# Performance work log

Measured on AMD Instinct MI355X. Metric: run time of the kernel, lower is better.

The kernel has to match this reference:

```python
import jax, jax.numpy as jnp
import numpy as np

N, E = 50000, 1600000
IN_CH, HEADS, OUT_PER_HEAD = 128, 4, 32  # out_channels=128 // 4 heads
NEG_SLOPE = 0.2


def setup_inputs() -> dict:
    key = jax.random.key(0)
    ks = jax.random.split(key, 10)
    HC = HEADS * OUT_PER_HEAD
    glorot = lambda k, shape: jax.random.uniform(k, shape, jnp.float32, -1.0, 1.0) * jnp.sqrt(6.0 / (shape[0] + shape[-1]))
    return {
        "x": jax.random.normal(ks[0], (N, IN_CH), jnp.float32),
        "edge_index": jax.random.randint(ks[1], (2, E), 0, N),
        "edge_weight": jax.random.uniform(ks[2], (E,), jnp.float32),
        "Wl": glorot(ks[3], (IN_CH, HC)),
        "bl": jnp.zeros((HC,), jnp.float32),
        "Wr": glorot(ks[4], (IN_CH, HC)),
        "br": jnp.zeros((HC,), jnp.float32),
        "We": glorot(ks[5], (1, HC)),           # lin_edge, bias=False
        "att": glorot(ks[6], (HEADS, OUT_PER_HEAD)),
        "bias": jnp.zeros((HC,), jnp.float32),
    }


def reference(x, edge_index, edge_weight, Wl, bl, Wr, br, We, att, bias):
    n = x.shape[0]
    H, C = att.shape
    src, dst = edge_index[0], edge_index[1]
    # add_self_loops with fill_value='max': self-loop edge_attr = max incoming edge weight per node (0 if none)
    loop_attr = jax.ops.segment_max(edge_weight, dst, num_segments=n)
    loop_attr = jnp.where(jnp.isfinite(loop_attr), loop_attr, 0.0)
    loop = jnp.arange(n)
    src_f = jnp.concatenate([src, loop])
    dst_f = jnp.concatenate([dst, loop])
    ea_f = jnp.concatenate([edge_weight, loop_attr])[:, None]  # [E+N, 1]
    # GATv2: separate src/dst linear transforms
    x_l = (x @ Wl + bl).reshape(n, H, C)
    x_r = (x @ Wr + br).reshape(n, H, C)
    e = (ea_f @ We).reshape(-1, H, C)
    # per-edge message and attention score
    m = jax.nn.leaky_relu(x_l[src_f] + x_r[dst_f] + e, NEG_SLOPE)  # [E+N, H, C]
    alpha = jnp.einsum('ehc,hc->eh', m, att)
    # scatter-softmax over incoming edges per destination node
    amax = jax.ops.segment_max(alpha, dst_f, num_segments=n)
    amax = jnp.where(jnp.isfinite(amax), amax, 0.0)
    aexp = jnp.exp(alpha - amax[dst_f])
    asum = jax.ops.segment_sum(aexp, dst_f, num_segments=n)
    alpha = aexp / (asum[dst_f] + 1e-16)
    # weighted aggregate of source-transformed features
    out = jax.ops.segment_sum(x_l[src_f] * alpha[..., None], dst_f, num_segments=n)
    return out.reshape(n, H * C) + bias
```

## Files before the change

kernel.cpp:

```cpp
#include <hip/hip_runtime.h>
#include <cstdint>

#define NEG 0.2f
#define BSH 4
#define BNODES 16
#define CAP 768
#define EPT 3
#define SBSH 9
#define SBN 512
#define CCAP 18000
#define CCHUNK 3328
#define CEPT 13
#define FSLICE 8
#define LOG2E 1.44269504088896f

typedef __attribute__((ext_vector_type(8))) short short8v;
typedef __attribute__((ext_vector_type(4))) float f32x4;

__device__ __forceinline__ unsigned short f2bf(float f) {
  unsigned u = __float_as_uint(f);
  return (unsigned short)((u + 0x7FFFu + ((u >> 16) & 1u)) >> 16);
}
__device__ __forceinline__ float bf2f(unsigned short h) {
  return __uint_as_float(((unsigned)h) << 16);
}

__global__ __launch_bounds__(256) void k_prep(const float* __restrict__ Wl,
    const float* __restrict__ Wr, const float* __restrict__ We,
    const float* __restrict__ att, unsigned short* __restrict__ WtB,
    float* __restrict__ qe) {
  int mat = blockIdx.x;
  const float* W = mat ? Wr : Wl;
  for (int i = threadIdx.x; i < 16384; i += 256) {
    int c = i >> 7, k = i & 127;
    WtB[mat * 16384 + c * 128 + k] = f2bf(W[k * 128 + c]);
  }
  if (mat == 0) {
    __shared__ float tmp[128];
    if (threadIdx.x < 128) tmp[threadIdx.x] = att[threadIdx.x] * We[threadIdx.x];
    __syncthreads();
    if (threadIdx.x < 4) {
      float s = 0.f;
      for (int c = 0; c < 32; ++c) s += tmp[threadIdx.x * 32 + c];
      qe[threadIdx.x] = 0.6f * LOG2E * s;
    }
  }
}

__global__ __launch_bounds__(256) void k_gemm(const float* __restrict__ x,
    const unsigned short* __restrict__ WtB, const float* __restrict__ att,
    const float* __restrict__ bl, const float* __restrict__ br,
    unsigned short* __restrict__ xlb, unsigned short* __restrict__ xrb,
    float* __restrict__ ql, float* __restrict__ qr, int n) {
  __shared__ __align__(16) unsigned short xs[64][136];
  __shared__ __align__(16) unsigned short Wt[128][136];
  int tid = threadIdx.x;
  int B0 = blockIdx.x * 64;
  int mat = blockIdx.y;
  for (int i = tid; i < 64 * 32; i += 256) {
    int r = i >> 5, c4 = (i & 31) * 4;
    ushort4 o = {0, 0, 0, 0};
    if (B0 + r < n) {
      float4 v = *(const float4*)(x + (size_t)(B0 + r) * 128 + c4);
      o = make_ushort4(f2bf(v.x), f2bf(v.y), f2bf(v.z), f2bf(v.w));
    }
    *(ushort4*)&xs[r][c4] = o;
  }
  for (int i = tid; i < 128 * 32; i += 256) {
    int c = i >> 5, k4 = (i & 31) * 4;
    *(ushort4*)&Wt[c][k4] = *(const ushort4*)(WtB + (size_t)mat * 16384 + c * 128 + k4);
  }
  __syncthreads();
  int wv = tid >> 6, lane = tid & 63;
  int l15 = lane & 15, g = lane >> 4;
  int R0 = wv * 16;
  f32x4 acc[8];
  #pragma unroll
  for (int t = 0; t < 8; ++t) acc[t] = {0.f, 0.f, 0.f, 0.f};
  #pragma unroll
  for (int kc = 0; kc < 4; ++kc) {
    int k0 = kc * 32 + g * 8;
    short8v b = *(const short8v*)&xs[R0 + l15][k0];
    #pragma unroll
    for (int t = 0; t < 8; ++t) {
      short8v a = *(const short8v*)&Wt[t * 16 + l15][k0];
      acc[t] = __builtin_amdgcn_mfma_f32_16x16x32_bf16(a, b, acc[t], 0, 0, 0);
    }
  }
  const float* bias = mat ? br : bl;
  unsigned short* yp = mat ? xrb : xlb;
  float* qdst = mat ? qr : ql;
  int row = B0 + R0 + l15;
  float qp[4] = {0.f, 0.f, 0.f, 0.f};
  if (row < n) {
    const float s06 = 0.6f * LOG2E;
    #pragma unroll
    for (int t = 0; t < 8; ++t) {
      int c0 = t * 16 + g * 4;
      float4 bv = *(const float4*)(bias + c0);
      float4 av = *(const float4*)(att + c0);
      ushort4 o = {f2bf(acc[t][0] + bv.x), f2bf(acc[t][1] + bv.y),
                   f2bf(acc[t][2] + bv.z), f2bf(acc[t][3] + bv.w)};
      *(ushort4*)(yp + (size_t)row * 128 + c0) = o;
      float dot = av.x * bf2f(o.x) + av.y * bf2f(o.y)
                + av.z * bf2f(o.z) + av.w * bf2f(o.w);
      qp[t >> 1] += s06 * dot;
    }
  }
  #pragma unroll
  for (int h = 0; h < 4; ++h) {
    qp[h] += __shfl_xor(qp[h], 16);
    qp[h] += __shfl_xor(qp[h], 32);
  }
  if (row < n && g == 0)
    *(float4*)(qdst + (size_t)row * 4) = make_float4(qp[0], qp[1], qp[2], qp[3]);
}

__global__ __launch_bounds__(256) void k_coarse(const int* __restrict__ eidx,
    const float* __restrict__ ew, unsigned* __restrict__ gsb,
    int2* __restrict__ csb, int E, int NSB) {
  __shared__ unsigned cnt[128];
  __shared__ unsigned base[128];
  int c0 = blockIdx.x * CCHUNK;
  int c1 = min(E, c0 + CCHUNK);
  if (c0 >= c1) return;
  for (int b = threadIdx.x; b < NSB; b += 256) cnt[b] = 0u;
  __syncthreads();
  unsigned dreg[CEPT];
  #pragma unroll
  for (int k = 0; k < CEPT; ++k) {
    int i = c0 + threadIdx.x + k * 256;
    unsigned d = 0u;
    if (i < c1) {
      d = (unsigned)eidx[E + i];
      atomicAdd(&cnt[d >> SBSH], 1u);
    }
    dreg[k] = d;
  }
  __syncthreads();
  for (int b = threadIdx.x; b < NSB; b += 256) {
    unsigned c = cnt[b];
    base[b] = c ? atomicAdd(&gsb[b], c) : 0u;
    cnt[b] = 0u;
  }
  __syncthreads();
  #pragma unroll
  for (int k = 0; k < CEPT; ++k) {
    int i = c0 + threadIdx.x + k * 256;
    if (i < c1) {
      unsigned d = dreg[k];
      unsigned b = d >> SBSH;
      unsigned slot = base[b] + atomicAdd(&cnt[b], 1u);
      if (slot < CCAP)
        csb[(size_t)b * CCAP + slot] =
            make_int2((eidx[i] << SBSH) | (int)(d & (SBN - 1)), __float_as_int(ew[i]));
    }
  }
}

__global__ __launch_bounds__(256) void k_fine(const unsigned* __restrict__ gsb,
    const int2* __restrict__ csb, int2* __restrict__ ebkt,
    unsigned* __restrict__ fcnt, int NB) {
  __shared__ unsigned cnt[32];
  __shared__ unsigned base[32];
  int sb = blockIdx.x / FSLICE;
  int sl = blockIdx.x % FSLICE;
  int ne = min((int)gsb[sb], CCAP);
  int chunk = (ne + FSLICE - 1) / FSLICE;
  int i0 = sl * chunk, i1 = min(ne, i0 + chunk);
  if (i0 >= i1) return;
  const int2* src = csb + (size_t)sb * CCAP;
  if (threadIdx.x < 32) cnt[threadIdx.x] = 0u;
  __syncthreads();
  for (int i = i0 + threadIdx.x; i < i1; i += 256)
    atomicAdd(&cnt[(src[i].x >> 4) & 31], 1u);
  __syncthreads();
  if (threadIdx.x < 32) {
    unsigned c = cnt[threadIdx.x];
    base[threadIdx.x] = c ? atomicAdd(&fcnt[sb * 32 + (int)threadIdx.x], c) : 0u;
    cnt[threadIdx.x] = 0u;
  }
  __syncthreads();
  for (int i = i0 + threadIdx.x; i < i1; i += 256) {
    int2 e = src[i];
    int fb = (e.x >> 4) & 31;
    unsigned slot = base[fb] + atomicAdd(&cnt[fb], 1u);
    if (slot < CAP) {
      int packed = ((e.x >> SBSH) << 4) | (e.x & 15);
      ebkt[(size_t)(sb * 32 + fb) * CAP + slot] = make_int2(packed, e.y);
    }
  }
}

__global__ __launch_bounds__(256) void k_agg(
    const unsigned* __restrict__ fcnt, const int2* __restrict__ ebkt,
    const unsigned short* __restrict__ xlb, const unsigned short* __restrict__ xrb,
    const float* __restrict__ ql, const float* __restrict__ qr,
    const float* __restrict__ qe, const float* __restrict__ We,
    const float* __restrict__ att, const float* __restrict__ bias,
    float* __restrict__ out, int n) {
  __shared__ int2 es[CAP];
  __shared__ unsigned rp[BNODES + 1];
  __shared__ unsigned cur[BNODES];
  __shared__ unsigned scnt[BNODES];
  int tid = threadIdx.x;
  int lane = tid & 63, wv = tid >> 6;
  int bkt = blockIdx.x;
  int ne = min((int)fcnt[bkt], CAP);
  const int2* srcp = ebkt + (size_t)bkt * CAP;
  if (tid < BNODES) scnt[tid] = 0u;
  __syncthreads();
  int2 er[EPT];
  #pragma unroll
  for (int k = 0; k < EPT; ++k) {
    int i = tid + k * 256;
    if (i < ne) {
      er[k] = srcp[i];
      atomicAdd(&scnt[er[k].x & (BNODES - 1)], 1u);
    }
  }
  __syncthreads();
  if (tid < 64) {
    unsigned s = (lane < BNODES) ? scnt[lane] : 0u;
    #pragma unroll
    for (int off = 1; off < BNODES; off <<= 1) {
      unsigned t = __shfl_up(s, off);
      if (lane >= off) s += t;
    }
    if (lane < BNODES) { rp[lane + 1] = s; cur[lane] = 0u; }
    if (lane == 0) rp[0] = 0u;
  }
  __syncthreads();
  #pragma unroll
  for (int k = 0; k < EPT; ++k) {
    int i = tid + k * 256;
    if (i < ne) {
      int dl = er[k].x & (BNODES - 1);
      unsigned slot = rp[dl] + atomicAdd(&cur[dl], 1u);
      es[slot] = make_int2(er[k].x >> BSH, er[k].y);
    }
  }
  __syncthreads();

  int g = lane >> 4;
  int l4 = lane & 15;
  int h = l4 >> 2;
  int ch0 = l4 * 8;
  float4 weA = *(const float4*)(We + ch0);
  float4 weB = *(const float4*)(We + ch0 + 4);
  float4 atA = *(const float4*)(att + ch0);
  float4 atB = *(const float4*)(att + ch0 + 4);
  const float s04 = 0.4f * LOG2E;
  atA.x *= s04; atA.y *= s04; atA.z *= s04; atA.w *= s04;
  atB.x *= s04; atB.y *= s04; atB.z *= s04; atB.w *= s04;
  float qeh = qe[h];

  for (int dl = wv; dl < BNODES; dl += 4) {
    int d = (bkt << BSH) + dl;
    if (d >= n) break;
    int s0 = (int)rp[dl], s1 = (int)rp[dl + 1];
    uint4 xrq = *(const uint4*)(xrb + ((size_t)d << 7) + ch0);
    float4 xrA, xrB;
    xrA.x = __uint_as_float(xrq.x << 16);
    xrA.y = __uint_as_float(xrq.x & 0xFFFF0000u);
    xrA.z = __uint_as_float(xrq.y << 16);
    xrA.w = __uint_as_float(xrq.y & 0xFFFF0000u);
    xrB.x = __uint_as_float(xrq.z << 16);
    xrB.y = __uint_as_float(xrq.z & 0xFFFF0000u);
    xrB.z = __uint_as_float(xrq.w << 16);
    xrB.w = __uint_as_float(xrq.w & 0xFFFF0000u);
    float qrd = qr[(size_t)d * 4 + h];
    float den = 0.f, wmax = -INFINITY;
    float4 aA = {0, 0, 0, 0}, aB = {0, 0, 0, 0};
    int idx = s0 + g;
    bool valid = idx < s1;
    int2 ev = make_int2(0, 0);
    uint4 xq = {0, 0, 0, 0};
    float qls = 0.f;
    if (valid) {
      ev = es[idx];
      xq = *(const uint4*)(xlb + ((size_t)ev.x << 7) + ch0);
      qls = ql[(size_t)ev.x * 4 + h];
    }
    for (int j = s0; j < s1; j += 4) {
      int idxn = j + 4 + g;
      bool vn = idxn < s1;
      int2 evn = ev; uint4 xqn = xq; float qln = qls;
      if (vn) {
        evn = es[idxn];
        xqn = *(const uint4*)(xlb + ((size_t)evn.x << 7) + ch0);
        qln = ql[(size_t)evn.x * 4 + h];
      }
      if (valid) {
        float w = __int_as_float(ev.y);
        wmax = fmaxf(wmax, w);
        float4 xA, xB;
        xA.x = __uint_as_float(xq.x << 16);
        xA.y = __uint_as_float(xq.x & 0xFFFF0000u);
        xA.z = __uint_as_float(xq.y << 16);
        xA.w = __uint_as_float(xq.y & 0xFFFF0000u);
        xB.x = __uint_as_float(xq.z << 16);
        xB.y = __uint_as_float(xq.z & 0xFFFF0000u);
        xB.z = __uint_as_float(xq.w << 16);
        xB.w = __uint_as_float(xq.w & 0xFFFF0000u);
        float nl = 0.f, t;
        t = xA.x + fmaf(w, weA.x, xrA.x); nl = fmaf(atA.x, fabsf(t), nl);
        t = xA.y + fmaf(w, weA.y, xrA.y); nl = fmaf(atA.y, fabsf(t), nl);
        t = xA.z + fmaf(w, weA.z, xrA.z); nl = fmaf(atA.z, fabsf(t), nl);
        t = xA.w + fmaf(w, weA.w, xrA.w); nl = fmaf(atA.w, fabsf(t), nl);
        t = xB.x + fmaf(w, weB.x, xrB.x); nl = fmaf(atB.x, fabsf(t), nl);
        t = xB.y + fmaf(w, weB.y, xrB.y); nl = fmaf(atB.y, fabsf(t), nl);
        t = xB.z + fmaf(w, weB.z, xrB.z); nl = fmaf(atB.z, fabsf(t), nl);
        t = xB.w + fmaf(w, weB.w, xrB.w); nl = fmaf(atB.w, fabsf(t), nl);
        nl += __shfl_xor(nl, 1);
        nl += __shfl_xor(nl, 2);
        float pe = exp2f(qls + fmaf(w, qeh, qrd) + nl);
        den += pe;
        aA.x += pe * xA.x; aA.y += pe * xA.y; aA.z += pe * xA.z; aA.w += pe * xA.w;
        aB.x += pe * xB.x; aB.y += pe * xB.y; aB.z += pe * xB.z; aB.w += pe * xB.w;
      }
      ev = evn; xq = xqn; qls = qln; valid = vn;
    }
    #pragma unroll
    for (int mask = 16; mask <= 32; mask <<= 1) {
      den += __shfl_xor(den, mask);
      aA.x += __shfl_xor(aA.x, mask); aA.y += __shfl_xor(aA.y, mask);
      aA.z += __shfl_xor(aA.z, mask); aA.w += __shfl_xor(aA.w, mask);
      aB.x += __shfl_xor(aB.x, mask); aB.y += __shfl_xor(aB.y, mask);
      aB.z += __shfl_xor(aB.z, mask); aB.w += __shfl_xor(aB.w, mask);
      wmax = fmaxf(wmax, __shfl_xor(wmax, mask));
    }
    {
      float wl = (wmax > -INFINITY) ? wmax : 0.f;
      uint4 xq2 = *(const uint4*)(xlb + ((size_t)d << 7) + ch0);
      float4 xA, xB;
      xA.x = __uint_as_float(xq2.x << 16);
      xA.y = __uint_as_float(xq2.x & 0xFFFF0000u);
      xA.z = __uint_as_float(xq2.y << 16);
      xA.w = __uint_as_float(xq2.y & 0xFFFF0000u);
      xB.x = __uint_as_float(xq2.z << 16);
      xB.y = __uint_as_float(xq2.z & 0xFFFF0000u);
      xB.z = __uint_as_float(xq2.w << 16);
      xB.w = __uint_as_float(xq2.w & 0xFFFF0000u);
      float nl = 0.f, t;
      t = xA.x + fmaf(wl, weA.x, xrA.x); nl = fmaf(atA.x, fabsf(t), nl);
      t = xA.y + fmaf(wl, weA.y, xrA.y); nl = fmaf(atA.y, fabsf(t), nl);
      t = xA.z + fmaf(wl, weA.z, xrA.z); nl = fmaf(atA.z, fabsf(t), nl);
      t = xA.w + fmaf(wl, weA.w, xrA.w); nl = fmaf(atA.w, fabsf(t), nl);
      t = xB.x + fmaf(wl, weB.x, xrB.x); nl = fmaf(atB.x, fabsf(t), nl);
      t = xB.y + fmaf(wl, weB.y, xrB.y); nl = fmaf(atB.y, fabsf(t), nl);
      t = xB.z + fmaf(wl, weB.z, xrB.z); nl = fmaf(atB.z, fabsf(t), nl);
      t = xB.w + fmaf(wl, weB.w, xrB.w); nl = fmaf(atB.w, fabsf(t), nl);
      nl += __shfl_xor(nl, 1);
      nl += __shfl_xor(nl, 2);
      float qld = ql[(size_t)d * 4 + h];
      float pe = exp2f(qld + fmaf(wl, qeh, qrd) + nl);
      den += pe;
      aA.x += pe * xA.x; aA.y += pe * xA.y; aA.z += pe * xA.z; aA.w += pe * xA.w;
      aB.x += pe * xB.x; aB.y += pe * xB.y; aB.z += pe * xB.z; aB.w += pe * xB.w;
    }
    if (g == 0) {
      float r = 1.0f / den;
      float4 bvA = *(const float4*)(bias + ch0);
      float4 bvB = *(const float4*)(bias + ch0 + 4);
      float* op = out + (size_t)d * 128 + ch0;
      float4 oA = {aA.x * r + bvA.x, aA.y * r + bvA.y, aA.z * r + bvA.z, aA.w * r + bvA.w};
      float4 oB = {aB.x * r + bvB.x, aB.y * r + bvB.y, aB.z * r + bvB.z, aB.w * r + bvB.w};
      *(float4*)op = oA;
      *(float4*)(op + 4) = oB;
    }
  }
}

extern "C" void kernel_launch(void* const* d_in, const int* in_sizes, int n_in,
                              void* d_out, int out_size, void* d_ws, size_t ws_size,
                              hipStream_t stream) {
  const float* x     = (const float*)d_in[0];
  const int*   eidx  = (const int*)d_in[1];
  const float* ew_in = (const float*)d_in[2];
  const float* Wl    = (const float*)d_in[3];
  const float* bl    = (const float*)d_in[4];
  const float* Wr    = (const float*)d_in[5];
  const float* br    = (const float*)d_in[6];
  const float* We    = (const float*)d_in[7];
  const float* att   = (const float*)d_in[8];
  const float* bias  = (const float*)d_in[9];
  float* out = (float*)d_out;

  const int N = in_sizes[0] / 128;
  const int E = in_sizes[2];
  const int NB = (N + BNODES - 1) >> BSH;
  const int NSB = (N + SBN - 1) >> SBSH;

  char* ws = (char*)d_ws;
  size_t off = 0;
  auto alloc = [&](size_t bytes) {
    void* p = ws + off;
    off = (off + bytes + 255) & ~(size_t)255;
    return p;
  };
  int2* ebkt = (int2*)alloc((size_t)NB * CAP * 8);
  size_t ov_start = off;
  unsigned short* xlb = (unsigned short*)alloc((size_t)N * 128 * 2);
  unsigned short* xrb = (unsigned short*)alloc((size_t)N * 128 * 2);
  int2* csb = (int2*)(ws + ov_start);
  unsigned short* WtB = (unsigned short*)alloc(2 * 16384 * 2);
  float* ql = (float*)alloc((size_t)N * 4 * 4);
  float* qr = (float*)alloc((size_t)N * 4 * 4);
  float* qe = (float*)alloc(4 * 4);
  unsigned* fcnt = (unsigned*)alloc((size_t)NB * 4);
  unsigned* gsb  = (unsigned*)alloc((size_t)NSB * 4);

  size_t z0 = (size_t)((char*)fcnt - ws);
  size_t z1 = (size_t)((char*)gsb - ws) + (size_t)NSB * 4;
  hipMemsetAsync(ws + z0, 0, z1 - z0, stream);

  k_prep<<<2, 256, 0, stream>>>(Wl, Wr, We, att, WtB, qe);

  int nblk = (E + CCHUNK - 1) / CCHUNK;
  k_coarse<<<nblk, 256, 0, stream>>>(eidx, ew_in, gsb, csb, E, NSB);

  k_fine<<<NSB * FSLICE, 256, 0, stream>>>(gsb, csb, ebkt, fcnt, NB);

  k_gemm<<<dim3((N + 63) / 64, 2), 256, 0, stream>>>(x, WtB, att, bl, br, xlb, xrb, ql, qr, N);

  k_agg<<<NB, 256, 0, stream>>>(fcnt, ebkt, xlb, xrb, ql, qr, qe, We, att, bias, out, N);
}
```

Before: 162.6 us.

## Drop fine bucketing pass; aggregate directly from 64-node coarse buckets

Removes the k_fine second-level bucketing kernel. The coarse pass now bins edges into 64-node buckets, and k_agg consumes those buckets directly with 512-thread blocks, doing the in-block counting sort over 64 destinations. The intent is to cut one kernel launch and a full read/write pass over the edge array. The trade-off is a coarse scatter over about 782 buckets with larger shared-memory histograms, which adds atomic contention and LDS use. It also switches exp2f to the hardware exp2 builtin.

```diff
diff --git a/kernel.cpp b/kernel.cpp
--- a/kernel.cpp
+++ b/kernel.cpp
@@ -2,16 +2,13 @@
 #include <cstdint>
 
 #define NEG 0.2f
-#define BSH 4
-#define BNODES 16
-#define CAP 768
-#define EPT 3
-#define SBSH 9
-#define SBN 512
-#define CCAP 18000
+#define SBSH 6
+#define BNODES 64
+#define CCAP 2400
+#define EPT 5
 #define CCHUNK 3328
 #define CEPT 13
-#define FSLICE 8
+#define MAXNSB 1024
 #define LOG2E 1.44269504088896f
 
 typedef __attribute__((ext_vector_type(8))) short short8v;
@@ -119,8 +116,8 @@
 __global__ __launch_bounds__(256) void k_coarse(const int* __restrict__ eidx,
     const float* __restrict__ ew, unsigned* __restrict__ gsb,
     int2* __restrict__ csb, int E, int NSB) {
-  __shared__ unsigned cnt[128];
-  __shared__ unsigned base[128];
+  __shared__ unsigned cnt[MAXNSB];
+  __shared__ unsigned base[MAXNSB];
   int c0 = blockIdx.x * CCHUNK;
   int c1 = min(E, c0 + CCHUNK);
   if (c0 >= c1) return;
@@ -153,67 +150,33 @@
       unsigned slot = base[b] + atomicAdd(&cnt[b], 1u);
       if (slot < CCAP)
         csb[(size_t)b * CCAP + slot] =
-            make_int2((eidx[i] << SBSH) | (int)(d & (SBN - 1)), __float_as_int(ew[i]));
-    }
-  }
-}
-
-__global__ __launch_bounds__(256) void k_fine(const unsigned* __restrict__ gsb,
-    const int2* __restrict__ csb, int2* __restrict__ ebkt,
-    unsigned* __restrict__ fcnt, int NB) {
-  __shared__ unsigned cnt[32];
-  __shared__ unsigned base[32];
-  int sb = blockIdx.x / FSLICE;
-  int sl = blockIdx.x % FSLICE;
-  int ne = min((int)gsb[sb], CCAP);
-  int chunk = (ne + FSLICE - 1) / FSLICE;
-  int i0 = sl * chunk, i1 = min(ne, i0 + chunk);
-  if (i0 >= i1) return;
-  const int2* src = csb + (size_t)sb * CCAP;
-  if (threadIdx.x < 32) cnt[threadIdx.x] = 0u;
-  __syncthreads();
-  for (int i = i0 + threadIdx.x; i < i1; i += 256)
-    atomicAdd(&cnt[(src[i].x >> 4) & 31], 1u);
-  __syncthreads();
-  if (threadIdx.x < 32) {
-    unsigned c = cnt[threadIdx.x];
-    base[threadIdx.x] = c ? atomicAdd(&fcnt[sb * 32 + (int)threadIdx.x], c) : 0u;
-    cnt[threadIdx.x] = 0u;
-  }
-  __syncthreads();
-  for (int i = i0 + threadIdx.x; i < i1; i += 256) {
-    int2 e = src[i];
-    int fb = (e.x >> 4) & 31;
-    unsigned slot = base[fb] + atomicAdd(&cnt[fb], 1u);
-    if (slot < CAP) {
-      int packed = ((e.x >> SBSH) << 4) | (e.x & 15);
-      ebkt[(size_t)(sb * 32 + fb) * CAP + slot] = make_int2(packed, e.y);
-    }
-  }
-}
-
-__global__ __launch_bounds__(256) void k_agg(
-    const unsigned* __restrict__ fcnt, const int2* __restrict__ ebkt,
+            make_int2((eidx[i] << SBSH) | (int)(d & (BNODES - 1)), __float_as_int(ew[i]));
+    }
+  }
+}
+
+__global__ __launch_bounds__(512) void k_agg(
+    const unsigned* __restrict__ gsb, const int2* __restrict__ csb,
     const unsigned short* __restrict__ xlb, const unsigned short* __restrict__ xrb,
     const float* __restrict__ ql, const float* __restrict__ qr,
     const float* __restrict__ qe, const float* __restrict__ We,
     const float* __restrict__ att, const float* __restrict__ bias,
     float* __restrict__ out, int n) {
-  __shared__ int2 es[CAP];
+  __shared__ int2 es[CCAP];
   __shared__ unsigned rp[BNODES + 1];
   __shared__ unsigned cur[BNODES];
   __shared__ unsigned scnt[BNODES];
   int tid = threadIdx.x;
   int lane = tid & 63, wv = tid >> 6;
-  int bkt = blockIdx.x;
-  int ne = min((int)fcnt[bkt], CAP);
-  const int2* srcp = ebkt + (size_t)bkt * CAP;
+  int sb = blockIdx.x;
+  int ne = min((int)gsb[sb], CCAP);
+  const int2* srcp = csb + (size_t)sb * CCAP;
   if (tid < BNODES) scnt[tid] = 0u;
   __syncthreads();
   int2 er[EPT];
   #pragma unroll
   for (int k = 0; k < EPT; ++k) {
-    int i = tid + k * 256;
+    int i = tid + k * 512;
     if (i < ne) {
       er[k] = srcp[i];
       atomicAdd(&scnt[er[k].x & (BNODES - 1)], 1u);
@@ -221,23 +184,24 @@
   }
   __syncthreads();
   if (tid < 64) {
-    unsigned s = (lane < BNODES) ? scnt[lane] : 0u;
+    unsigned s = scnt[lane];
     #pragma unroll
-    for (int off = 1; off < BNODES; off <<= 1) {
+    for (int off = 1; off < 64; off <<= 1) {
       unsigned t = __shfl_up(s, off);
       if (lane >= off) s += t;
     }
-    if (lane < BNODES) { rp[lane + 1] = s; cur[lane] = 0u; }
+    rp[lane + 1] = s;
+    cur[lane] = 0u;
     if (lane == 0) rp[0] = 0u;
   }
   __syncthreads();
   #pragma unroll
   for (int k = 0; k < EPT; ++k) {
-    int i = tid + k * 256;
+    int i = tid + k * 512;
     if (i < ne) {
       int dl = er[k].x & (BNODES - 1);
       unsigned slot = rp[dl] + atomicAdd(&cur[dl], 1u);
-      es[slot] = make_int2(er[k].x >> BSH, er[k].y);
+      es[slot] = make_int2(er[k].x >> SBSH, er[k].y);
     }
   }
   __syncthreads();
@@ -255,8 +219,8 @@
   atB.x *= s04; atB.y *= s04; atB.z *= s04; atB.w *= s04;
   float qeh = qe[h];
 
-  for (int dl = wv; dl < BNODES; dl += 4) {
-    int d = (bkt << BSH) + dl;
+  for (int dl = wv; dl < BNODES; dl += 8) {
+    int d = (sb << SBSH) + dl;
     if (d >= n) break;
     int s0 = (int)rp[dl], s1 = (int)rp[dl + 1];
     uint4 xrq = *(const uint4*)(xrb + ((size_t)d << 7) + ch0);
@@ -314,7 +278,7 @@
         t = xB.w + fmaf(w, weB.w, xrB.w); nl = fmaf(atB.w, fabsf(t), nl);
         nl += __shfl_xor(nl, 1);
         nl += __shfl_xor(nl, 2);
-        float pe = exp2f(qls + fmaf(w, qeh, qrd) + nl);
+        float pe = __builtin_amdgcn_exp2f(qls + fmaf(w, qeh, qrd) + nl);
         den += pe;
         aA.x += pe * xA.x; aA.y += pe * xA.y; aA.z += pe * xA.z; aA.w += pe * xA.w;
         aB.x += pe * xB.x; aB.y += pe * xB.y; aB.z += pe * xB.z; aB.w += pe * xB.w;
@@ -354,7 +318,7 @@
       nl += __shfl_xor(nl, 1);
       nl += __shfl_xor(nl, 2);
       float qld = ql[(size_t)d * 4 + h];
-      float pe = exp2f(qld + fmaf(wl, qeh, qrd) + nl);
+      float pe = __builtin_amdgcn_exp2f(qld + fmaf(wl, qeh, qrd) + nl);
       den += pe;
       aA.x += pe * xA.x; aA.y += pe * xA.y; aA.z += pe * xA.z; aA.w += pe * xA.w;
       aB.x += pe * xB.x; aB.y += pe * xB.y; aB.z += pe * xB.z; aB.w += pe * xB.w;
@@ -389,8 +353,7 @@
 
   const int N = in_sizes[0] / 128;
   const int E = in_sizes[2];
-  const int NB = (N + BNODES - 1) >> BSH;
-  const int NSB = (N + SBN - 1) >> SBSH;
+  const int NSB = (N + BNODES - 1) >> SBSH;
 
   char* ws = (char*)d_ws;
   size_t off = 0;
@@ -399,30 +362,23 @@
     off = (off + bytes + 255) & ~(size_t)255;
     return p;
   };
-  int2* ebkt = (int2*)alloc((size_t)NB * CAP * 8);
-  size_t ov_start = off;
+  int2* csb = (int2*)alloc((size_t)NSB * CCAP * 8);
   unsigned short* xlb = (unsigned short*)alloc((size_t)N * 128 * 2);
   unsigned short* xrb = (unsigned short*)alloc((size_t)N * 128 * 2);
-  int2* csb = (int2*)(ws + ov_start);
   unsigned short* WtB = (unsigned short*)alloc(2 * 16384 * 2);
   float* ql = (float*)alloc((size_t)N * 4 * 4);
   float* qr = (float*)alloc((size_t)N * 4 * 4);
   float* qe = (float*)alloc(4 * 4);
-  unsigned* fcnt = (unsigned*)alloc((size_t)NB * 4);
-  unsigned* gsb  = (unsigned*)alloc((size_t)NSB * 4);
-
-  size_t z0 = (size_t)((char*)fcnt - ws);
-  size_t z1 = (size_t)((char*)gsb - ws) + (size_t)NSB * 4;
-  hipMemsetAsync(ws + z0, 0, z1 - z0, stream);
+  unsigned* gsb = (unsigned*)alloc((size_t)NSB * 4);
+
+  hipMemsetAsync(gsb, 0, (size_t)NSB * 4, stream);
 
   k_prep<<<2, 256, 0, stream>>>(Wl, Wr, We, att, WtB, qe);
 
   int nblk = (E + CCHUNK - 1) / CCHUNK;
   k_coarse<<<nblk, 256, 0, stream>>>(eidx, ew_in, gsb, csb, E, NSB);
 
-  k_fine<<<NSB * FSLICE, 256, 0, stream>>>(gsb, csb, ebkt, fcnt, NB);
-
   k_gemm<<<dim3((N + 63) / 64, 2), 256, 0, stream>>>(x, WtB, att, bl, br, xlb, xrb, ql, qr, N);
 
-  k_agg<<<NB, 256, 0, stream>>>(fcnt, ebkt, xlb, xrb, ql, qr, qe, We, att, bias, out, N);
-}
+  k_agg<<<NSB, 512, 0, stream>>>(gsb, csb, xlb, xrb, ql, qr, qe, We, att, bias, out, N);
+}
```

Result: slower. 173.0 us (+6.4%).
